# Performance work log

Measured on AMD Instinct MI355X. Metric: run time of the kernel, lower is better.

## Reference

```python
import jax, jax.numpy as jnp
import numpy as np

D_INNER, D_STATE, DT_RANK = 2048, 16, 128
BATCH, SEQ = 2, 2048


def setup_inputs() -> dict:
    key = jax.random.key(0)
    ks = jax.random.split(key, 6)
    x = jax.random.normal(ks[0], (BATCH, SEQ, D_INNER), dtype=jnp.float32)
    # A_log initialized uniform(-4, -1) per _init_parameters
    A_log = jax.random.uniform(ks[1], (D_INNER, D_STATE), minval=-4.0, maxval=-1.0, dtype=jnp.float32)
    D = jnp.ones((D_INNER,), dtype=jnp.float32)
    # torch Linear weights: [out_features, in_features], kaiming-uniform-ish scale
    x_proj_w = jax.random.normal(ks[2], (DT_RANK + 2 * D_STATE, D_INNER), dtype=jnp.float32) / np.sqrt(D_INNER)
    dt_proj_w = jax.random.normal(ks[3], (D_INNER, DT_RANK), dtype=jnp.float32) / np.sqrt(DT_RANK)
    dt_std = DT_RANK ** (-0.5)
    dt_proj_b = jax.random.uniform(ks[4], (D_INNER,), minval=-dt_std, maxval=dt_std, dtype=jnp.float32)
    return {"x": x, "A_log": A_log, "D": D, "x_proj_w": x_proj_w,
            "dt_proj_w": dt_proj_w, "dt_proj_b": dt_proj_b}


def _selective_scan(u, delta, A, B, C, D):
    # u, delta: [b, l, d]; A: [d, n]; B, C: [b, l, n]; D: [d]
    dA = jnp.exp(delta[..., None] * A[None, None])          # [b, l, d, n]
    dBu = (delta * u)[..., None] * B[:, :, None, :]         # [b, l, d, n]

    def step(h, inp):
        dA_t, dBu_t, C_t = inp                              # [b,d,n],[b,d,n],[b,n]
        h = dA_t * h + dBu_t
        y_t = jnp.einsum('bdn,bn->bd', h, C_t)
        return h, y_t

    h0 = jnp.zeros((u.shape[0], u.shape[2], A.shape[1]), dtype=u.dtype)
    xs = (jnp.moveaxis(dA, 1, 0), jnp.moveaxis(dBu, 1, 0), jnp.moveaxis(C, 1, 0))
    _, ys = jax.lax.scan(step, h0, xs)                      # ys: [l, b, d]
    y = jnp.moveaxis(ys, 0, 1)
    return y + u * D[None, None, :]


def reference(x, A_log, D, x_proj_w, dt_proj_w, dt_proj_b):
    # x: [b, l, d_inner]
    x_dbl = jnp.einsum('bld,ed->ble', x, x_proj_w)          # [b, l, dt_rank + 2n]
    delta_r = x_dbl[..., :DT_RANK]
    B = x_dbl[..., DT_RANK:DT_RANK + D_STATE]
    C = x_dbl[..., DT_RANK + D_STATE:]
    delta = jnp.einsum('blr,dr->bld', delta_r, dt_proj_w) + dt_proj_b
    delta = jax.nn.softplus(delta)                          # delta_softplus=True
    A = -jnp.exp(A_log)
    return _selective_scan(x, delta, A, B, C, D)
```

## Files before the change

### kernel.cpp

```cpp
#include <hip/hip_runtime.h>
#include <math.h>

#define DI   2048
#define DS   16
#define DTR  128
#define NBATCH 2
#define SEQ  2048
#define ROWS (NBATCH*SEQ)
#define NE   (DTR + 2*DS)
#define NC   32
#define LC   (SEQ/NC)
#define KS1  8

typedef float f32x4 __attribute__((ext_vector_type(4)));
typedef short s16x8 __attribute__((ext_vector_type(8)));
typedef short s16x4 __attribute__((ext_vector_type(4)));

__device__ inline short f2bf(float f) {
    unsigned u = __builtin_bit_cast(unsigned, f);
    u += 0x7FFFu + ((u >> 16) & 1u);
    return (short)(u >> 16);
}

__global__ __launch_bounds__(256) void k_castw(const float* __restrict__ w,
                                               const float* __restrict__ dtw,
                                               short* __restrict__ wb,
                                               short* __restrict__ dtwb) {
    int i = blockIdx.x*256 + threadIdx.x;
    if (i < 81920) {
        float4 v = ((const float4*)w)[i];
        s16x4 o = { f2bf(v.x), f2bf(v.y), f2bf(v.z), f2bf(v.w) };
        *(s16x4*)(wb + 4*i) = o;
    } else if (i < 147456) {
        int j = i - 81920;
        float4 v = ((const float4*)dtw)[j];
        s16x4 o = { f2bf(v.x), f2bf(v.y), f2bf(v.z), f2bf(v.w) };
        *(s16x4*)(dtwb + 4*j) = o;
    }
}

__global__ __launch_bounds__(256) void k_gemm1(const float* __restrict__ x,
                                               const short* __restrict__ wb,
                                               float* __restrict__ part) {
    const int wave = blockIdx.x*4 + (threadIdx.x >> 6);
    const int lane = threadIdx.x & 63;
    const int m16 = wave & 255;
    const int ks  = wave >> 8;
    const int r = lane & 15, g = lane >> 4;
    f32x4 acc[10];
    #pragma unroll
    for (int i = 0; i < 10; i++) acc[i] = (f32x4){0.f,0.f,0.f,0.f};

    const float* xp = x + (size_t)(m16*16 + r)*DI + g*8;
    #pragma unroll 2
    for (int kk = 0; kk < 8; ++kk) {
        const int k0 = ks*256 + kk*32;
        float4 xa = *(const float4*)(xp + k0);
        float4 xc = *(const float4*)(xp + k0 + 4);
        s16x8 afrag = { f2bf(xa.x), f2bf(xa.y), f2bf(xa.z), f2bf(xa.w),
                        f2bf(xc.x), f2bf(xc.y), f2bf(xc.z), f2bf(xc.w) };
        const short* bp = wb + (size_t)r*DI + k0 + g*8;
        #pragma unroll
        for (int nf = 0; nf < 10; ++nf) {
            s16x8 bfrag = *(const s16x8*)(bp + (size_t)nf*16*DI);
            acc[nf] = __builtin_amdgcn_mfma_f32_16x16x32_bf16(afrag, bfrag, acc[nf], 0, 0, 0);
        }
    }
    const int orow = m16*16 + g*4;
    #pragma unroll
    for (int nf = 0; nf < 10; ++nf)
        #pragma unroll
        for (int j = 0; j < 4; ++j)
            part[((size_t)ks*ROWS + orow + j)*NE + nf*16 + r] = acc[nf][j];
}

__global__ __launch_bounds__(256) void k_split(const float* __restrict__ part,
                                               short* __restrict__ dRb,
                                               float* __restrict__ Bm,
                                               float* __restrict__ Cm) {
    int i = blockIdx.x*256 + threadIdx.x;
    if (i >= ROWS*NE) return;
    float v = 0.f;
    #pragma unroll
    for (int s = 0; s < KS1; ++s) v += part[(size_t)s*ROWS*NE + i];
    int row = i / NE, e = i - row*NE;
    if (e < DTR)            dRb[(size_t)row*DTR + e] = f2bf(v);
    else if (e < DTR + DS)  Bm[(size_t)row*DS + (e - DTR)] = v;
    else                    Cm[(size_t)row*DS + (e - DTR - DS)] = v;
}

__global__ __launch_bounds__(256) void k_gemm2(const short* __restrict__ dRb,
                                               const short* __restrict__ dtwb,
                                               const float* __restrict__ bias,
                                               float* __restrict__ delta) {
    const int wave = blockIdx.x*4 + (threadIdx.x >> 6);
    const int lane = threadIdx.x & 63;
    const int m16 = wave >> 5, nt = wave & 31;
    const int r = lane & 15, g = lane >> 4;

    s16x8 a[4];
    const short* ap = dRb + (size_t)(m16*16 + r)*DTR + g*8;
    #pragma unroll
    for (int ks = 0; ks < 4; ++ks) a[ks] = *(const s16x8*)(ap + ks*32);

    f32x4 acc[4];
    #pragma unroll
    for (int i = 0; i < 4; i++) acc[i] = (f32x4){0.f,0.f,0.f,0.f};

    #pragma unroll
    for (int nf = 0; nf < 4; ++nf) {
        const short* bp = dtwb + (size_t)(nt*64 + nf*16 + r)*DTR + g*8;
        #pragma unroll
        for (int ks = 0; ks < 4; ++ks) {
            s16x8 b = *(const s16x8*)(bp + ks*32);
            acc[nf] = __builtin_amdgcn_mfma_f32_16x16x32_bf16(a[ks], b, acc[nf], 0, 0, 0);
        }
    }
    const int orow = m16*16 + g*4;
    #pragma unroll
    for (int nf = 0; nf < 4; ++nf) {
        const int col = nt*64 + nf*16 + r;
        const float bb = bias[col];
        #pragma unroll
        for (int j = 0; j < 4; ++j) {
            float v = acc[nf][j] + bb;
            delta[(size_t)(orow + j)*DI + col] = fmaxf(v, 0.f) + log1pf(__expf(-fabsf(v)));
        }
    }
}

__global__ __launch_bounds__(256) void k_scan1(const float* __restrict__ delta,
                                               const float* __restrict__ x,
                                               const float* __restrict__ Bm,
                                               const float* __restrict__ A_log,
                                               float* __restrict__ aprod,
                                               float* __restrict__ rsum) {
    const int tid  = threadIdx.x;
    const int lane = tid & 63;
    const int w    = blockIdx.x*4 + (tid >> 6);
    const int dlow = lane & 15, q = lane >> 4;
    const int d16  = w & 127;
    const int rest = w >> 7;
    const int b = rest & 1, c = rest >> 1;
    const int d = d16*16 + dlow;
    const int n0 = 4*q;

    float4 Alg = *(const float4*)(A_log + (size_t)d*DS + n0);
    float An[4] = { -__expf(Alg.x), -__expf(Alg.y), -__expf(Alg.z), -__expf(Alg.w) };
    float ap[4] = {1.f,1.f,1.f,1.f}, r[4] = {0.f,0.f,0.f,0.f};

    const float* dp = delta + (size_t)b*SEQ*DI + d;
    const float* xp = x     + (size_t)b*SEQ*DI + d;
    const float* bp = Bm    + (size_t)b*SEQ*DS + n0;
    const int lbase = c*LC;
    #pragma unroll 2
    for (int tt = 0; tt < LC; ++tt) {
        const int l = lbase + tt;
        float dlt = dp[(size_t)l*DI];
        float u   = xp[(size_t)l*DI];
        float du  = dlt * u;
        float4 bv = *(const float4*)(bp + (size_t)l*DS);
        float bb[4] = {bv.x, bv.y, bv.z, bv.w};
        #pragma unroll
        for (int j = 0; j < 4; ++j) {
            float da = __expf(dlt * An[j]);
            r[j]  = fmaf(da, r[j], du * bb[j]);
            ap[j] *= da;
        }
    }
    size_t base = (((size_t)c*NBATCH + b)*DI + d)*DS + n0;
    *(float4*)(aprod + base) = (float4){ap[0], ap[1], ap[2], ap[3]};
    *(float4*)(rsum  + base) = (float4){r[0],  r[1],  r[2],  r[3]};
}

__global__ __launch_bounds__(256) void k_mid(const float* __restrict__ aprod,
                                             const float* __restrict__ rsum,
                                             float* __restrict__ hin) {
    int gid = blockIdx.x*256 + threadIdx.x;
    int n = gid & 15;
    int d = (gid >> 4) & (DI-1);
    int b = gid >> 15;
    float h = 0.f;
    for (int c = 0; c < NC; c++) {
        size_t idx = (((size_t)c*NBATCH + b)*DI + d)*DS + n;
        hin[idx] = h;
        h = fmaf(aprod[idx], h, rsum[idx]);
    }
}

__global__ __launch_bounds__(256) void k_scan2(const float* __restrict__ delta,
                                               const float* __restrict__ x,
                                               const float* __restrict__ Bm,
                                               const float* __restrict__ Cm,
                                               const float* __restrict__ A_log,
                                               const float* __restrict__ Dv,
                                               const float* __restrict__ hin,
                                               float* __restrict__ y) {
    const int tid  = threadIdx.x;
    const int lane = tid & 63;
    const int w    = blockIdx.x*4 + (tid >> 6);
    const int dlow = lane & 15, q = lane >> 4;
    const int d16  = w & 127;
    const int rest = w >> 7;
    const int b = rest & 1, c = rest >> 1;
    const int d = d16*16 + dlow;
    const int n0 = 4*q;

    float4 Alg = *(const float4*)(A_log + (size_t)d*DS + n0);
    float An[4] = { -__expf(Alg.x), -__expf(Alg.y), -__expf(Alg.z), -__expf(Alg.w) };
    size_t base = (((size_t)c*NBATCH + b)*DI + d)*DS + n0;
    float4 hv = *(const float4*)(hin + base);
    float h[4] = {hv.x, hv.y, hv.z, hv.w};

    const float Dd = Dv[d];
    const float* dp = delta + (size_t)b*SEQ*DI + d;
    const float* xp = x     + (size_t)b*SEQ*DI + d;
    const float* bp = Bm    + (size_t)b*SEQ*DS + n0;
    const float* cp = Cm    + (size_t)b*SEQ*DS + n0;
    float* yp = y + (size_t)b*SEQ*DI + d;
    const int lbase = c*LC;
    #pragma unroll 2
    for (int tt = 0; tt < LC; ++tt) {
        const int l = lbase + tt;
        float dlt = dp[(size_t)l*DI];
        float u   = xp[(size_t)l*DI];
        float du  = dlt * u;
        float4 bv = *(const float4*)(bp + (size_t)l*DS);
        float4 cv = *(const float4*)(cp + (size_t)l*DS);
        float bb[4] = {bv.x, bv.y, bv.z, bv.w};
        float cc[4] = {cv.x, cv.y, cv.z, cv.w};
        float acc = 0.f;
        #pragma unroll
        for (int j = 0; j < 4; ++j) {
            float da = __expf(dlt * An[j]);
            h[j] = fmaf(da, h[j], du * bb[j]);
            acc  = fmaf(h[j], cc[j], acc);
        }
        acc += __shfl_xor(acc, 16);
        acc += __shfl_xor(acc, 32);
        if (q == 0) yp[(size_t)l*DI] = fmaf(u, Dd, acc);
    }
}

extern "C" void kernel_launch(void* const* d_in, const int* in_sizes, int n_in,
                              void* d_out, int out_size, void* d_ws, size_t ws_size,
                              hipStream_t stream) {
    const float* x     = (const float*)d_in[0];
    const float* A_log = (const float*)d_in[1];
    const float* Dv    = (const float*)d_in[2];
    const float* xpw   = (const float*)d_in[3];
    const float* dtw   = (const float*)d_in[4];
    const float* dtb   = (const float*)d_in[5];
    float* out = (float*)d_out;

    const size_t SCN = (size_t)NC*NBATCH*DS*DI;

    float* ws    = (float*)d_ws;
    float* delta = ws;
    float* unionR= delta + (size_t)ROWS*DI;
    float* part  = unionR;
    float* aprod = unionR;
    float* rsum  = aprod + SCN;
    float* hin   = rsum  + SCN;
    float* uend  = unionR + ((3*SCN > (size_t)KS1*ROWS*NE) ? 3*SCN : (size_t)KS1*ROWS*NE);
    float* Bm    = uend;
    float* Cm    = Bm + (size_t)ROWS*DS;
    short* dRb   = (short*)(Cm + (size_t)ROWS*DS);
    short* wb    = dRb + (size_t)ROWS*DTR;
    short* dtwb  = wb  + (size_t)160*2048;

    k_castw<<<576, 256, 0, stream>>>(xpw, dtw, wb, dtwb);
    k_gemm1<<<512, 256, 0, stream>>>(x, wb, part);
    k_split<<<(ROWS*NE + 255)/256, 256, 0, stream>>>(part, dRb, Bm, Cm);
    k_gemm2<<<2048, 256, 0, stream>>>(dRb, dtwb, dtb, delta);
    k_scan1<<<2048, 256, 0, stream>>>(delta, x, Bm, A_log, aprod, rsum);
    k_mid<<<256, 256, 0, stream>>>(aprod, rsum, hin);
    k_scan2<<<2048, 256, 0, stream>>>(delta, x, Bm, Cm, A_log, Dv, hin, out);
}
```

Measured before the change: 227.9 us.

## Stage scan inputs in LDS per chunk; use packed bf16 convert and fast log

Both scan kernels now use one block per 64-channel slice and sequence chunk. The block cooperatively loads the delta, x, B and C tiles for the chunk into shared memory with coalesced float4 loads, then runs the recurrence from LDS. Before, each thread did strided per-timestep global loads. The GEMM1 A-fragment conversion uses the packed bf16x2 intrinsic, and softplus uses __logf instead of log1pf. These add LDS usage and a block barrier, and slightly change softplus precision for small values.

New measurement: 211.8 us. 1.08x faster.

```diff
diff --git a/kernel.cpp b/kernel.cpp
--- a/kernel.cpp
+++ b/kernel.cpp
@@ -1,4 +1,5 @@
 #include <hip/hip_runtime.h>
+#include <hip/hip_bf16.h>
 #include <math.h>
 
 #define DI   2048
@@ -20,6 +21,12 @@
     unsigned u = __builtin_bit_cast(unsigned, f);
     u += 0x7FFFu + ((u >> 16) & 1u);
     return (short)(u >> 16);
+}
+
+__device__ inline unsigned pk2(float lo, float hi) {
+    union { __hip_bfloat162 h; unsigned u; } cv;
+    cv.h = __float22bfloat162_rn(float2{lo, hi});
+    return cv.u;
 }
 
 __global__ __launch_bounds__(256) void k_castw(const float* __restrict__ w,
@@ -57,13 +64,16 @@
         const int k0 = ks*256 + kk*32;
         float4 xa = *(const float4*)(xp + k0);
         float4 xc = *(const float4*)(xp + k0 + 4);
-        s16x8 afrag = { f2bf(xa.x), f2bf(xa.y), f2bf(xa.z), f2bf(xa.w),
-                        f2bf(xc.x), f2bf(xc.y), f2bf(xc.z), f2bf(xc.w) };
+        union { s16x8 v; unsigned u[4]; } af;
+        af.u[0] = pk2(xa.x, xa.y);
+        af.u[1] = pk2(xa.z, xa.w);
+        af.u[2] = pk2(xc.x, xc.y);
+        af.u[3] = pk2(xc.z, xc.w);
         const short* bp = wb + (size_t)r*DI + k0 + g*8;
         #pragma unroll
         for (int nf = 0; nf < 10; ++nf) {
             s16x8 bfrag = *(const s16x8*)(bp + (size_t)nf*16*DI);
-            acc[nf] = __builtin_amdgcn_mfma_f32_16x16x32_bf16(afrag, bfrag, acc[nf], 0, 0, 0);
+            acc[nf] = __builtin_amdgcn_mfma_f32_16x16x32_bf16(af.v, bfrag, acc[nf], 0, 0, 0);
         }
     }
     const int orow = m16*16 + g*4;
@@ -124,7 +134,8 @@
         #pragma unroll
         for (int j = 0; j < 4; ++j) {
             float v = acc[nf][j] + bb;
-            delta[(size_t)(orow + j)*DI + col] = fmaxf(v, 0.f) + log1pf(__expf(-fabsf(v)));
+            delta[(size_t)(orow + j)*DI + col] =
+                fmaxf(v, 0.f) + __logf(1.f + __expf(-fabsf(v)));
         }
     }
 }
@@ -135,36 +146,52 @@
                                                const float* __restrict__ A_log,
                                                float* __restrict__ aprod,
                                                float* __restrict__ rsum) {
-    const int tid  = threadIdx.x;
-    const int lane = tid & 63;
-    const int w    = blockIdx.x*4 + (tid >> 6);
+    __shared__ float ld[LC][64];
+    __shared__ float lx[LC][64];
+    __shared__ float lB[LC][DS];
+    const int tid = threadIdx.x;
+    const int bb = blockIdx.x & 31;
+    const int b  = (blockIdx.x >> 5) & 1;
+    const int c  = blockIdx.x >> 6;
+    const int d0 = bb*64;
+    const int lbase = c*LC;
+
+    {
+        const float* dsrc = delta + ((size_t)(b*SEQ + lbase))*DI + d0;
+        const float* xsrc = x     + ((size_t)(b*SEQ + lbase))*DI + d0;
+        const int row = tid >> 4, col = (tid & 15)*4;
+        #pragma unroll
+        for (int i = 0; i < 4; i++) {
+            *(float4*)&ld[row + 16*i][col] = *(const float4*)(dsrc + (size_t)(row + 16*i)*DI + col);
+            *(float4*)&lx[row + 16*i][col] = *(const float4*)(xsrc + (size_t)(row + 16*i)*DI + col);
+        }
+        const float* bsrc = Bm + ((size_t)(b*SEQ + lbase))*DS;
+        *(float4*)&lB[tid >> 2][(tid & 3)*4] = *(const float4*)(bsrc + tid*4);
+    }
+
+    const int lane = tid & 63, widx = tid >> 6;
     const int dlow = lane & 15, q = lane >> 4;
-    const int d16  = w & 127;
-    const int rest = w >> 7;
-    const int b = rest & 1, c = rest >> 1;
-    const int d = d16*16 + dlow;
+    const int dcol = widx*16 + dlow;
+    const int d = d0 + dcol;
     const int n0 = 4*q;
 
     float4 Alg = *(const float4*)(A_log + (size_t)d*DS + n0);
     float An[4] = { -__expf(Alg.x), -__expf(Alg.y), -__expf(Alg.z), -__expf(Alg.w) };
     float ap[4] = {1.f,1.f,1.f,1.f}, r[4] = {0.f,0.f,0.f,0.f};
 
-    const float* dp = delta + (size_t)b*SEQ*DI + d;
-    const float* xp = x     + (size_t)b*SEQ*DI + d;
-    const float* bp = Bm    + (size_t)b*SEQ*DS + n0;
-    const int lbase = c*LC;
-    #pragma unroll 2
+    __syncthreads();
+
+    #pragma unroll 8
     for (int tt = 0; tt < LC; ++tt) {
-        const int l = lbase + tt;
-        float dlt = dp[(size_t)l*DI];
-        float u   = xp[(size_t)l*DI];
+        float dlt = ld[tt][dcol];
+        float u   = lx[tt][dcol];
         float du  = dlt * u;
-        float4 bv = *(const float4*)(bp + (size_t)l*DS);
-        float bb[4] = {bv.x, bv.y, bv.z, bv.w};
+        float4 bv = *(const float4*)&lB[tt][n0];
+        float bbv[4] = {bv.x, bv.y, bv.z, bv.w};
         #pragma unroll
         for (int j = 0; j < 4; ++j) {
             float da = __expf(dlt * An[j]);
-            r[j]  = fmaf(da, r[j], du * bb[j]);
+            r[j]  = fmaf(da, r[j], du * bbv[j]);
             ap[j] *= da;
         }
     }
@@ -196,14 +223,36 @@
                                                const float* __restrict__ Dv,
                                                const float* __restrict__ hin,
                                                float* __restrict__ y) {
-    const int tid  = threadIdx.x;
-    const int lane = tid & 63;
-    const int w    = blockIdx.x*4 + (tid >> 6);
+    __shared__ float ld[LC][64];
+    __shared__ float lx[LC][64];
+    __shared__ float lB[LC][DS];
+    __shared__ float lC[LC][DS];
+    const int tid = threadIdx.x;
+    const int bb = blockIdx.x & 31;
+    const int b  = (blockIdx.x >> 5) & 1;
+    const int c  = blockIdx.x >> 6;
+    const int d0 = bb*64;
+    const int lbase = c*LC;
+
+    {
+        const float* dsrc = delta + ((size_t)(b*SEQ + lbase))*DI + d0;
+        const float* xsrc = x     + ((size_t)(b*SEQ + lbase))*DI + d0;
+        const int row = tid >> 4, col = (tid & 15)*4;
+        #pragma unroll
+        for (int i = 0; i < 4; i++) {
+            *(float4*)&ld[row + 16*i][col] = *(const float4*)(dsrc + (size_t)(row + 16*i)*DI + col);
+            *(float4*)&lx[row + 16*i][col] = *(const float4*)(xsrc + (size_t)(row + 16*i)*DI + col);
+        }
+        const float* bsrc = Bm + ((size_t)(b*SEQ + lbase))*DS;
+        const float* csrc = Cm + ((size_t)(b*SEQ + lbase))*DS;
+        *(float4*)&lB[tid >> 2][(tid & 3)*4] = *(const float4*)(bsrc + tid*4);
+        *(float4*)&lC[tid >> 2][(tid & 3)*4] = *(const float4*)(csrc + tid*4);
+    }
+
+    const int lane = tid & 63, widx = tid >> 6;
     const int dlow = lane & 15, q = lane >> 4;
-    const int d16  = w & 127;
-    const int rest = w >> 7;
-    const int b = rest & 1, c = rest >> 1;
-    const int d = d16*16 + dlow;
+    const int dcol = widx*16 + dlow;
+    const int d = d0 + dcol;
     const int n0 = 4*q;
 
     float4 Alg = *(const float4*)(A_log + (size_t)d*DS + n0);
@@ -211,34 +260,30 @@
     size_t base = (((size_t)c*NBATCH + b)*DI + d)*DS + n0;
     float4 hv = *(const float4*)(hin + base);
     float h[4] = {hv.x, hv.y, hv.z, hv.w};
-
     const float Dd = Dv[d];
-    const float* dp = delta + (size_t)b*SEQ*DI + d;
-    const float* xp = x     + (size_t)b*SEQ*DI + d;
-    const float* bp = Bm    + (size_t)b*SEQ*DS + n0;
-    const float* cp = Cm    + (size_t)b*SEQ*DS + n0;
-    float* yp = y + (size_t)b*SEQ*DI + d;
-    const int lbase = c*LC;
-    #pragma unroll 2
+    float* yp = y + ((size_t)(b*SEQ + lbase))*DI + d;
+
+    __syncthreads();
+
+    #pragma unroll 8
     for (int tt = 0; tt < LC; ++tt) {
-        const int l = lbase + tt;
-        float dlt = dp[(size_t)l*DI];
-        float u   = xp[(size_t)l*DI];
+        float dlt = ld[tt][dcol];
+        float u   = lx[tt][dcol];
         float du  = dlt * u;
-        float4 bv = *(const float4*)(bp + (size_t)l*DS);
-        float4 cv = *(const float4*)(cp + (size_t)l*DS);
-        float bb[4] = {bv.x, bv.y, bv.z, bv.w};
-        float cc[4] = {cv.x, cv.y, cv.z, cv.w};
+        float4 bv = *(const float4*)&lB[tt][n0];
+        float4 cv = *(const float4*)&lC[tt][n0];
+        float bbv[4] = {bv.x, bv.y, bv.z, bv.w};
+        float ccv[4] = {cv.x, cv.y, cv.z, cv.w};
         float acc = 0.f;
         #pragma unroll
         for (int j = 0; j < 4; ++j) {
             float da = __expf(dlt * An[j]);
-            h[j] = fmaf(da, h[j], du * bb[j]);
-            acc  = fmaf(h[j], cc[j], acc);
+            h[j] = fmaf(da, h[j], du * bbv[j]);
+            acc  = fmaf(h[j], ccv[j], acc);
         }
         acc += __shfl_xor(acc, 16);
         acc += __shfl_xor(acc, 32);
-        if (q == 0) yp[(size_t)l*DI] = fmaf(u, Dd, acc);
+        if (q == 0) yp[(size_t)tt*DI] = fmaf(u, Dd, acc);
     }
 }
 
```
